# Kernel optimization log

Measured on AMD Instinct MI355X. Metric: run time of the kernel, lower is better.

## Reference

```python
import jax, jax.numpy as jnp
import numpy as np

# Dimensions (see shape_source): batch, tokens, input dim, attention feature dim, output dim
B, T, D_IN, D_ATTN, D_OUT = 8, 2048, 512, 8, 512
# Weight scale keeps Q,K entries ~N(0, 0.5^2) so scores**power stays finite in fp32
W_SCALE = 0.5 / np.sqrt(D_IN)


def setup_inputs() -> dict:
    key = jax.random.key(0)
    k1, k2, k3, k4 = jax.random.split(key, 4)
    Input = jax.random.normal(k1, (B, T, D_IN), dtype=jnp.float32)
    W_q = jax.random.normal(k2, (D_IN, D_ATTN), dtype=jnp.float32) * W_SCALE
    W_k = jax.random.normal(k3, (D_IN, D_ATTN), dtype=jnp.float32) * W_SCALE
    W_v = jax.random.normal(k4, (D_IN, D_OUT), dtype=jnp.float32) * W_SCALE
    return {"Input": Input, "W_q": W_q, "W_k": W_k, "W_v": W_v, "power": D_ATTN}


def reference(Input, W_q, W_k, W_v, power):
    # QKV projections (torch.mm applied per token)
    Q = jnp.einsum('btd,df->btf', Input, W_q)   # [B,T,D_ATTN]
    K = jnp.einsum('btd,df->btf', Input, W_k)   # [B,T,D_ATTN]
    V = jnp.einsum('btd,do->bto', Input, W_v)   # [B,T,D_OUT]
    # Non-standard score transform: elementwise power by Attention.Feature.Num
    scores = jnp.einsum('btf,bsf->bts', Q, K) ** power  # [B,T,T]
    A = jax.nn.softmax(scores, axis=2)
    # Weighted sum of values
    return jnp.einsum('bts,bso->bto', A, V)  # [B,T,D_OUT]
```

## Files before the change

### kernel.cpp

```cpp
#include <hip/hip_runtime.h>
#include <hip/hip_bf16.h>
#include <stdint.h>


typedef float f32x4_t __attribute__((ext_vector_type(4)));
typedef short s16x8_t __attribute__((ext_vector_type(8)));
typedef unsigned int u32;

static __device__ __forceinline__ unsigned short f2bf(float x){
  union { float f; u32 u; } v; v.f = x;
  return (unsigned short)((v.u + 0x7FFFu + ((v.u >> 16) & 1u)) >> 16);
}

static __device__ __forceinline__ u32 pk2bf(float a, float b){
  __hip_bfloat162 h = __float22bfloat162_rn(float2{a, b});
  union { __hip_bfloat162 h2; u32 u; } c; c.h2 = h;
  return c.u;
}

static __device__ __forceinline__ void gload16(const void* g, void* l){
  __builtin_amdgcn_global_load_lds((const __attribute__((address_space(1))) u32*)g,
                                   (__attribute__((address_space(3))) u32*)l, 16, 0, 0);
}

static __device__ __forceinline__ float dot8(const float* q, const float4& a, const float4& b){
  float s = q[0] * a.x;
  s = fmaf(q[1], a.y, s); s = fmaf(q[2], a.z, s); s = fmaf(q[3], a.w, s);
  s = fmaf(q[4], b.x, s); s = fmaf(q[5], b.y, s); s = fmaf(q[6], b.z, s);
  s = fmaf(q[7], b.w, s);
  return s;
}

__global__ __launch_bounds__(256) void k_wvT(const float* __restrict__ Wv,
                                             unsigned short* __restrict__ WvT){
  __shared__ __align__(16) float tile[64][68];
  const int t = threadIdx.x;
  const int dbase = (blockIdx.x >> 3) * 64;
  const int cbase = (blockIdx.x & 7) * 64;
  {
    const int dl = t >> 2, cq = (t & 3) * 16;
    const float* src = Wv + (size_t)(dbase + dl) * 512 + cbase + cq;
#pragma unroll
    for (int i = 0; i < 16; i += 4){
      float4 v = *(const float4*)(src + i);
      tile[dl][cq + i + 0] = v.x; tile[dl][cq + i + 1] = v.y;
      tile[dl][cq + i + 2] = v.z; tile[dl][cq + i + 3] = v.w;
    }
  }
  __syncthreads();
  const int cl = t >> 2, dq = (t & 3) * 16;
  __align__(16) unsigned short o[16];
#pragma unroll
  for (int i = 0; i < 16; ++i) o[i] = f2bf(tile[dq + i][cl]);
  unsigned short* dst = WvT + (size_t)(cbase + cl) * 512 + dbase + dq;
  *(uint4*)dst = *(const uint4*)o;
  *(uint4*)(dst + 8) = *(const uint4*)(o + 8);
}

__global__ __launch_bounds__(256) void k_fused(const float* __restrict__ In,
                                               const float* __restrict__ Wq,
                                               const float* __restrict__ Wk,
                                               const unsigned short* __restrict__ WvT,
                                               float* __restrict__ Qo,
                                               float* __restrict__ Ko,
                                               unsigned short* __restrict__ Vg){
  __shared__ __align__(16) char smem[65536];
  const int t = threadIdx.x;
  if (blockIdx.x < 1024){
    float* wt = (float*)smem;
    float* inT = (float*)(smem + 32768);
    const float* Inb = In + (size_t)blockIdx.x * 16 * 512;
#pragma unroll
    for (int i = 0; i < 8; ++i)
      gload16(Inb + (i * 256 + t) * 4, (char*)inT + (i * 256 + t) * 16);
#pragma unroll
    for (int i = 0; i < 16; i += 4){
      float4 vq = *(const float4*)(Wq + t * 16 + i);
      float4 vk = *(const float4*)(Wk + t * 16 + i);
      const float* pq = &vq.x;
      const float* pk = &vk.x;
#pragma unroll
      for (int j = 0; j < 4; ++j){
        int flat = t * 16 + i + j;
        int d = flat >> 3, f = flat & 7;
        wt[f * 512 + ((((d >> 2) ^ f) << 2) | (d & 3))] = pq[j];
        int fk = f + 8;
        wt[fk * 512 + ((((d >> 2) ^ (fk & 7)) << 2) | (d & 3))] = pk[j];
      }
    }
    __syncthreads();
    const int tokl = t >> 4;
    const int f = t & 15;
    const float* inrow = inT + tokl * 512;
    const float* wrow = &wt[f * 512];
    const int swz = f & 7;
    double acc = 0.0;
    for (int cb = 0; cb < 128; cb += 8){
      float part = 0.f;
#pragma unroll
      for (int c = cb; c < cb + 8; ++c){
        float4 x = *(const float4*)(inrow + c * 4);
        float4 ww = *(const float4*)(wrow + ((c ^ swz) << 2));
        part = fmaf(x.x, ww.x, part); part = fmaf(x.y, ww.y, part);
        part = fmaf(x.z, ww.z, part); part = fmaf(x.w, ww.w, part);
      }
      acc += (double)part;
    }
    float r = (float)acc;
    const int tok = (int)blockIdx.x * 16 + tokl;
    if (f < 8) Qo[(size_t)tok * 8 + f] = r;
    else       Ko[(size_t)tok * 8 + (f - 8)] = r;
    return;
  }
  char* Ab = smem;
  char* Bb = smem + 16384;
  char* Img = smem + 32768;
  const int vb = (int)blockIdx.x - 1024;
  const int w = t >> 6, lane = t & 63;
  const int mt = vb >> 2, nt = vb & 3;
  const int wm = w >> 1, wn = w & 1;
  const int asub = lane & 3;
  int arow[2], acr[2];
#pragma unroll
  for (int i = 0; i < 2; ++i){
    arow[i] = (w * 2 + i) * 16 + (lane >> 2);
    acr[i]  = asub ^ ((arow[i] >> 1) & 3);
  }
  f32x4_t acc[4][4];
#pragma unroll
  for (int m = 0; m < 4; ++m)
#pragma unroll
    for (int n = 0; n < 4; ++n)
      acc[m][n] = (f32x4_t){0.f, 0.f, 0.f, 0.f};

  auto stageB = [&](int kk, int sel){
#pragma unroll
    for (int i = 0; i < 2; ++i){
      int id = w * 2 + i;
      const unsigned short* gb = WvT + (size_t)(nt * 128 + arow[i]) * 512 + kk * 32 + acr[i] * 8;
      gload16(gb, Bb + sel * 8192 + id * 1024);
    }
  };
  auto loadA = [&](int kk, float4* x, float4* y){
#pragma unroll
    for (int i = 0; i < 2; ++i){
      const float* ga = In + (size_t)(mt * 128 + arow[i]) * 512 + kk * 32 + acr[i] * 8;
      x[i] = *(const float4*)ga;
      y[i] = *(const float4*)(ga + 4);
    }
  };
  auto writeA = [&](const float4* x, const float4* y, int sel){
#pragma unroll
    for (int i = 0; i < 2; ++i){
      __align__(16) unsigned short pk[8] = {
        f2bf(x[i].x), f2bf(x[i].y), f2bf(x[i].z), f2bf(x[i].w),
        f2bf(y[i].x), f2bf(y[i].y), f2bf(y[i].z), f2bf(y[i].w)};
      *(uint4*)(Ab + sel * 8192 + arow[i] * 64 + asub * 16) = *(const uint4*)pk;
    }
  };
  {
    float4 x[2], y[2];
    loadA(0, x, y);
    stageB(0, 0);
    writeA(x, y, 0);
    __syncthreads();
  }
  for (int kk = 0; kk < 16; ++kk){
    const int cur = kk & 1;
    float4 x[2], y[2];
    if (kk < 15){
      loadA(kk + 1, x, y);
      stageB(kk + 1, cur ^ 1);
    }
    s16x8_t a[4], bf[4];
#pragma unroll
    for (int m = 0; m < 4; ++m){
      int row = wm * 64 + m * 16 + (lane & 15);
      int chn = (lane >> 4) ^ ((row >> 1) & 3);
      a[m] = *(const s16x8_t*)(Ab + cur * 8192 + row * 64 + chn * 16);
    }
#pragma unroll
    for (int n = 0; n < 4; ++n){
      int col = wn * 64 + n * 16 + (lane & 15);
      int chn = (lane >> 4) ^ ((col >> 1) & 3);
      bf[n] = *(const s16x8_t*)(Bb + cur * 8192 + col * 64 + chn * 16);
    }
#pragma unroll
    for (int m = 0; m < 4; ++m)
#pragma unroll
      for (int n = 0; n < 4; ++n)
        acc[m][n] = __builtin_amdgcn_mfma_f32_16x16x32_bf16(a[m], bf[n], acc[m][n], 0, 0, 0);
    if (kk < 15) writeA(x, y, cur ^ 1);
    __syncthreads();
  }
#pragma unroll
  for (int m = 0; m < 4; ++m){
    const int ks2 = (wm * 2 + (m >> 1)) & 3;
    const int hi  = (m * 2 + ((lane >> 4) >> 1)) & 3;
    const int lo0 = ((lane >> 4) & 1) * 4;
#pragma unroll
    for (int n = 0; n < 4; ++n){
      const int g_loc = wn * 2 + (n >> 1);
      const int n2 = n & 1;
      const int cl = lane & 15;
      __align__(8) unsigned short pk2[4];
#pragma unroll
      for (int j = 0; j < 4; ++j) pk2[j] = f2bf(acc[m][n][j]);
      int boff = g_loc * 8192 + n2 * 4096 + ks2 * 1024 + hi * 256 + cl * 16 + lo0 * 2;
      *(uint2*)(Img + boff) = *(const uint2*)pk2;
    }
  }
  __syncthreads();
  const int bq = mt >> 4;
  const int kt = mt & 15;
#pragma unroll
  for (int i = 0; i < 8; ++i){
    int G = i * 256 + t;
    unsigned short* dst = Vg + (size_t)bq * 1048576 + (size_t)kt * 65536
                        + nt * 16384 + G * 8;
    *(uint4*)dst = *(const uint4*)(Img + G * 16);
  }
}

__global__ __launch_bounds__(1024) void k_attn(const float* __restrict__ Qg,
                                               const float* __restrict__ Kg,
                                               const unsigned short* __restrict__ Vg,
                                               float* __restrict__ Out){
  __shared__ __align__(16) char smem[102656];
  const int t = threadIdx.x;
  const int g = t >> 6, lane = t & 63;
  const int b = blockIdx.x & 7;
  const int qt = blockIdx.x >> 3;
  const int qbase = qt * 64;

  float qreg[8];
  {
    const float* Qp = Qg + (size_t)(b * 2048 + qbase + lane) * 8;
    float4 a = *(const float4*)Qp;
    float4 c = *(const float4*)(Qp + 4);
    qreg[0] = a.x; qreg[1] = a.y; qreg[2] = a.z; qreg[3] = a.w;
    qreg[4] = c.x; qreg[5] = c.y; qreg[6] = c.z; qreg[7] = c.w;
  }
  const float* Kp = Kg + (size_t)b * (2048 * 8);
  const unsigned short* Vb = Vg + (size_t)b * 1048576;
  char* Klds = smem;
  char* Pb = smem + 65536;
  float* red = (float*)(smem + 98304);
  float* fin = (float*)(smem + 102400);

#pragma unroll
  for (int i = 0; i < 4; ++i)
    gload16(Kp + (size_t)(i * 1024 + t) * 4, Klds + (i * 1024 + t) * 16);
  __syncthreads();

  float amax2 = 0.f;
  {
    const float* kbase = (const float*)Klds + (g * 8) * 8;
#pragma unroll 2
    for (int tt = 0; tt < 16; ++tt){
      const float* kb = kbase + tt * 1024;
#pragma unroll
      for (int j = 0; j < 8; ++j){
        float4 k0 = *(const float4*)(kb + j * 8);
        float4 k1 = *(const float4*)(kb + j * 8 + 4);
        float s = dot8(qreg, k0, k1);
        amax2 = fmaxf(amax2, s * s);
      }
    }
  }
  red[g * 64 + lane] = amax2;
  __syncthreads();
  float am = red[lane];
#pragma unroll
  for (int s = 1; s < 16; ++s) am = fmaxf(am, red[s * 64 + lane]);
  float mreg;
  { float s4 = am * am; mreg = s4 * s4; }
  const float LOG2E = 1.44269504f;
  const float me2 = mreg * LOG2E;
  float lp = 0.f;

  const int pswz = ((g ^ (lane & 15)) << 4);

  f32x4_t acc[4][2];
#pragma unroll
  for (int mm = 0; mm < 4; ++mm)
#pragma unroll
    for (int n = 0; n < 2; ++n)
      acc[mm][n] = (f32x4_t){0.f, 0.f, 0.f, 0.f};

  auto score_full = [&](int tt, int sel){
    const float* kb = (const float*)Klds + (tt * 128 + g * 8) * 8;
    uint4 pkd; u32* pw = &pkd.x;
#pragma unroll
    for (int jp = 0; jp < 4; ++jp){
      float e0, e1;
#pragma unroll
      for (int h = 0; h < 2; ++h){
        const int j = jp * 2 + h;
        float4 k0 = *(const float4*)(kb + j * 8);
        float4 k1 = *(const float4*)(kb + j * 8 + 4);
        float s = dot8(qreg, k0, k1);
        float s2 = s * s; float s4 = s2 * s2; float p = s4 * s4;
        float e = __builtin_amdgcn_exp2f(fmaf(p, LOG2E, -me2));
        lp += e;
        if (h == 0) e0 = e; else e1 = e;
      }
      pw[jp] = pk2bf(e0, e1);
    }
    *(uint4*)(Pb + sel * 16384 + lane * 256 + pswz) = pkd;
  };

  score_full(0, 0);
  __syncthreads();

  for (int tt = 0; tt < 16; ++tt){
    const int sel = tt & 1;
    s16x8_t vf[2][4];
    {
      const unsigned short* vb = Vb + (size_t)tt * 65536 + g * 4096 + lane * 8;
#pragma unroll
      for (int n = 0; n < 2; ++n)
#pragma unroll
        for (int ks = 0; ks < 4; ++ks)
          vf[n][ks] = *(const s16x8_t*)(vb + n * 2048 + ks * 512);
    }
    const bool more = (tt + 1 < 16);
    const float* kb = (const float*)Klds + (((tt + 1) & 15) * 128 + g * 8) * 8;
    uint4 pkd; u32* pw = &pkd.x;
#pragma unroll
    for (int ks = 0; ks < 4; ++ks){
      if (more){
        float e0, e1;
#pragma unroll
        for (int h = 0; h < 2; ++h){
          const int j = ks * 2 + h;
          float4 k0 = *(const float4*)(kb + j * 8);
          float4 k1 = *(const float4*)(kb + j * 8 + 4);
          float s = dot8(qreg, k0, k1);
          float s2 = s * s; float s4 = s2 * s2; float p = s4 * s4;
          float e = __builtin_amdgcn_exp2f(fmaf(p, LOG2E, -me2));
          lp += e;
          if (h == 0) e0 = e; else e1 = e;
        }
        pw[ks] = pk2bf(e0, e1);
      }
      s16x8_t a[4];
#pragma unroll
      for (int mm = 0; mm < 4; ++mm){
        int r = mm * 16 + (lane & 15);
        int slot = (ks * 4 + (lane >> 4)) ^ (r & 15);
        a[mm] = *(const s16x8_t*)(Pb + sel * 16384 + r * 256 + (slot << 4));
      }
      __builtin_amdgcn_s_setprio(1);
#pragma unroll
      for (int mm = 0; mm < 4; ++mm)
#pragma unroll
        for (int n = 0; n < 2; ++n)
          acc[mm][n] = __builtin_amdgcn_mfma_f32_16x16x32_bf16(a[mm], vf[n][ks], acc[mm][n], 0, 0, 0);
      __builtin_amdgcn_s_setprio(0);
    }
    if (more)
      *(uint4*)(Pb + (sel ^ 1) * 16384 + lane * 256 + pswz) = pkd;
    __syncthreads();
  }

  red[g * 64 + lane] = lp;
  __syncthreads();
  if (t < 64){
    float s = red[t];
#pragma unroll
    for (int s2 = 1; s2 < 16; ++s2) s += red[s2 * 64 + t];
    fin[t] = 1.f / s;
  }
  __syncthreads();

  float* img = (float*)smem;
#pragma unroll
  for (int mm = 0; mm < 4; ++mm){
    float linv[4];
#pragma unroll
    for (int j = 0; j < 4; ++j)
      linv[j] = fin[mm * 16 + ((lane >> 4) << 2) + j];
#pragma unroll
    for (int n = 0; n < 2; ++n){
      int colL = g * 32 + n * 16 + (lane & 15);
#pragma unroll
      for (int j = 0; j < 4; ++j){
        int r16 = ((lane >> 4) << 2) + j;
        img[r16 * 520 + colL] = acc[mm][n][j] * linv[j];
      }
    }
    __syncthreads();
#pragma unroll
    for (int i = 0; i < 2; ++i){
      int f4 = i * 1024 + t;
      int r16 = f4 >> 7, c4 = f4 & 127;
      float4 v = *(const float4*)(img + r16 * 520 + c4 * 4);
      *(float4*)(Out + (size_t)(b * 2048 + qbase + mm * 16 + r16) * 512 + c4 * 4) = v;
    }
    __syncthreads();
  }
}

extern "C" void kernel_launch(void* const* d_in, const int* in_sizes, int n_in,
                              void* d_out, int out_size, void* d_ws, size_t ws_size,
                              hipStream_t stream){
  const float* In = (const float*)d_in[0];
  const float* Wq = (const float*)d_in[1];
  const float* Wk = (const float*)d_in[2];
  const float* Wv = (const float*)d_in[3];
  char* ws = (char*)d_ws;
  unsigned short* WvT = (unsigned short*)(ws);
  float* Q            = (float*)(ws + 524288);
  float* K            = (float*)(ws + 1048576);
  unsigned short* Vg  = (unsigned short*)(ws + 1572864);
  float* Out = (float*)d_out;

  hipLaunchKernelGGL(k_wvT,   dim3(64),   dim3(256),  0, stream, Wv, WvT);
  hipLaunchKernelGGL(k_fused, dim3(1536), dim3(256),  0, stream, In, Wq, Wk, WvT, Q, K, Vg);
  hipLaunchKernelGGL(k_attn,  dim3(256),  dim3(1024), 0, stream, Q, K, Vg, Out);
}
```

Measured before the change: 99.17 us.

## Transpose K layout and vectorize score computation with packed FMA

The projection kernel now writes K in a feature-major tiled layout of 128 keys per tile, so each attention lane can read four consecutive keys per feature with one float4 LDS load. Scores are then computed two keys at a time using packed f32x2 FMAs (v_pk_fma_f32), and the power, exp-argument and row-sum steps are vectorized the same way. The intent is to cut VALU instruction count and LDS load count in the score-bound inner loop. Score computation is regrouped into two calls per tile instead of one per k-step, which changes how it interleaves with the MFMAs.

```diff
diff --git a/kernel.cpp b/kernel.cpp
--- a/kernel.cpp
+++ b/kernel.cpp
@@ -4,6 +4,7 @@
 
 
 typedef float f32x4_t __attribute__((ext_vector_type(4)));
+typedef float f32x2_t __attribute__((ext_vector_type(2)));
 typedef short s16x8_t __attribute__((ext_vector_type(8)));
 typedef unsigned int u32;
 
@@ -23,12 +24,8 @@
                                    (__attribute__((address_space(3))) u32*)l, 16, 0, 0);
 }
 
-static __device__ __forceinline__ float dot8(const float* q, const float4& a, const float4& b){
-  float s = q[0] * a.x;
-  s = fmaf(q[1], a.y, s); s = fmaf(q[2], a.z, s); s = fmaf(q[3], a.w, s);
-  s = fmaf(q[4], b.x, s); s = fmaf(q[5], b.y, s); s = fmaf(q[6], b.z, s);
-  s = fmaf(q[7], b.w, s);
-  return s;
+static __device__ __forceinline__ f32x2_t pfma(f32x2_t a, f32x2_t b, f32x2_t c){
+  return __builtin_elementwise_fma(a, b, c);
 }
 
 __global__ __launch_bounds__(256) void k_wvT(const float* __restrict__ Wv,
@@ -62,7 +59,7 @@
                                                const float* __restrict__ Wk,
                                                const unsigned short* __restrict__ WvT,
                                                float* __restrict__ Qo,
-                                               float* __restrict__ Ko,
+                                               float* __restrict__ Kt,
                                                unsigned short* __restrict__ Vg){
   __shared__ __align__(16) char smem[65536];
   const int t = threadIdx.x;
@@ -109,7 +106,10 @@
     float r = (float)acc;
     const int tok = (int)blockIdx.x * 16 + tokl;
     if (f < 8) Qo[(size_t)tok * 8 + f] = r;
-    else       Ko[(size_t)tok * 8 + (f - 8)] = r;
+    else {
+      const int bq = tok >> 11, kk = tok & 2047;
+      Kt[(size_t)bq * 16384 + (size_t)(kk >> 7) * 1024 + (f - 8) * 128 + (kk & 127)] = r;
+    }
     return;
   }
   char* Ab = smem;
@@ -223,7 +223,7 @@
 }
 
 __global__ __launch_bounds__(1024) void k_attn(const float* __restrict__ Qg,
-                                               const float* __restrict__ Kg,
+                                               const float* __restrict__ Kt,
                                                const unsigned short* __restrict__ Vg,
                                                float* __restrict__ Out){
   __shared__ __align__(16) char smem[102656];
@@ -233,15 +233,17 @@
   const int qt = blockIdx.x >> 3;
   const int qbase = qt * 64;
 
-  float qreg[8];
+  f32x2_t qq[8];
   {
     const float* Qp = Qg + (size_t)(b * 2048 + qbase + lane) * 8;
     float4 a = *(const float4*)Qp;
     float4 c = *(const float4*)(Qp + 4);
-    qreg[0] = a.x; qreg[1] = a.y; qreg[2] = a.z; qreg[3] = a.w;
-    qreg[4] = c.x; qreg[5] = c.y; qreg[6] = c.z; qreg[7] = c.w;
-  }
-  const float* Kp = Kg + (size_t)b * (2048 * 8);
+    qq[0] = (f32x2_t){a.x, a.x}; qq[1] = (f32x2_t){a.y, a.y};
+    qq[2] = (f32x2_t){a.z, a.z}; qq[3] = (f32x2_t){a.w, a.w};
+    qq[4] = (f32x2_t){c.x, c.x}; qq[5] = (f32x2_t){c.y, c.y};
+    qq[6] = (f32x2_t){c.z, c.z}; qq[7] = (f32x2_t){c.w, c.w};
+  }
+  const float* Kp = Kt + (size_t)b * 16384;
   const unsigned short* Vb = Vg + (size_t)b * 1048576;
   char* Klds = smem;
   char* Pb = smem + 65536;
@@ -255,16 +257,21 @@
 
   float amax2 = 0.f;
   {
-    const float* kbase = (const float*)Klds + (g * 8) * 8;
+    const float* kbase = (const float*)Klds + g * 8;
 #pragma unroll 2
     for (int tt = 0; tt < 16; ++tt){
       const float* kb = kbase + tt * 1024;
 #pragma unroll
-      for (int j = 0; j < 8; ++j){
-        float4 k0 = *(const float4*)(kb + j * 8);
-        float4 k1 = *(const float4*)(kb + j * 8 + 4);
-        float s = dot8(qreg, k0, k1);
-        amax2 = fmaxf(amax2, s * s);
+      for (int j = 0; j < 2; ++j){
+        f32x2_t p0 = {0.f, 0.f}, p1 = {0.f, 0.f};
+#pragma unroll
+        for (int d = 0; d < 8; ++d){
+          float4 v = *(const float4*)(kb + d * 128 + j * 4);
+          p0 = pfma(qq[d], (f32x2_t){v.x, v.y}, p0);
+          p1 = pfma(qq[d], (f32x2_t){v.z, v.w}, p1);
+        }
+        f32x2_t s0 = p0 * p0, s1 = p1 * p1;
+        amax2 = fmaxf(amax2, fmaxf(fmaxf(s0.x, s0.y), fmaxf(s1.x, s1.y)));
       }
     }
   }
@@ -276,8 +283,9 @@
   float mreg;
   { float s4 = am * am; mreg = s4 * s4; }
   const float LOG2E = 1.44269504f;
-  const float me2 = mreg * LOG2E;
-  float lp = 0.f;
+  const f32x2_t l2e  = (f32x2_t){LOG2E, LOG2E};
+  const f32x2_t nme2 = (f32x2_t){-mreg * LOG2E, -mreg * LOG2E};
+  f32x2_t lpp = (f32x2_t){0.f, 0.f};
 
   const int pswz = ((g ^ (lane & 15)) << 4);
 
@@ -288,29 +296,33 @@
     for (int n = 0; n < 2; ++n)
       acc[mm][n] = (f32x4_t){0.f, 0.f, 0.f, 0.f};
 
-  auto score_full = [&](int tt, int sel){
-    const float* kb = (const float*)Klds + (tt * 128 + g * 8) * 8;
-    uint4 pkd; u32* pw = &pkd.x;
-#pragma unroll
-    for (int jp = 0; jp < 4; ++jp){
-      float e0, e1;
-#pragma unroll
-      for (int h = 0; h < 2; ++h){
-        const int j = jp * 2 + h;
-        float4 k0 = *(const float4*)(kb + j * 8);
-        float4 k1 = *(const float4*)(kb + j * 8 + 4);
-        float s = dot8(qreg, k0, k1);
-        float s2 = s * s; float s4 = s2 * s2; float p = s4 * s4;
-        float e = __builtin_amdgcn_exp2f(fmaf(p, LOG2E, -me2));
-        lp += e;
-        if (h == 0) e0 = e; else e1 = e;
-      }
-      pw[jp] = pk2bf(e0, e1);
-    }
-    *(uint4*)(Pb + sel * 16384 + lane * 256 + pswz) = pkd;
+  auto score4 = [&](const float* kb, int j, u32* pw){
+    f32x2_t p0 = {0.f, 0.f}, p1 = {0.f, 0.f};
+#pragma unroll
+    for (int d = 0; d < 8; ++d){
+      float4 v = *(const float4*)(kb + d * 128 + j * 4);
+      p0 = pfma(qq[d], (f32x2_t){v.x, v.y}, p0);
+      p1 = pfma(qq[d], (f32x2_t){v.z, v.w}, p1);
+    }
+    p0 = p0 * p0; p1 = p1 * p1;
+    p0 = p0 * p0; p1 = p1 * p1;
+    p0 = p0 * p0; p1 = p1 * p1;
+    p0 = pfma(p0, l2e, nme2); p1 = pfma(p1, l2e, nme2);
+    float e0 = __builtin_amdgcn_exp2f(p0.x), e1 = __builtin_amdgcn_exp2f(p0.y);
+    float e2 = __builtin_amdgcn_exp2f(p1.x), e3 = __builtin_amdgcn_exp2f(p1.y);
+    lpp += (f32x2_t){e0, e1};
+    lpp += (f32x2_t){e2, e3};
+    pw[0] = pk2bf(e0, e1);
+    pw[1] = pk2bf(e2, e3);
   };
 
-  score_full(0, 0);
+  {
+    const float* kb0 = (const float*)Klds + g * 8;
+    uint4 pkd;
+    score4(kb0, 0, &pkd.x);
+    score4(kb0, 1, &pkd.z);
+    *(uint4*)(Pb + 0 * 16384 + lane * 256 + pswz) = pkd;
+  }
   __syncthreads();
 
   for (int tt = 0; tt < 16; ++tt){
@@ -325,25 +337,12 @@
           vf[n][ks] = *(const s16x8_t*)(vb + n * 2048 + ks * 512);
     }
     const bool more = (tt + 1 < 16);
-    const float* kb = (const float*)Klds + (((tt + 1) & 15) * 128 + g * 8) * 8;
-    uint4 pkd; u32* pw = &pkd.x;
+    const float* kbn = (const float*)Klds + ((tt + 1) & 15) * 1024 + g * 8;
+    uint4 pkd;
 #pragma unroll
     for (int ks = 0; ks < 4; ++ks){
-      if (more){
-        float e0, e1;
-#pragma unroll
-        for (int h = 0; h < 2; ++h){
-          const int j = ks * 2 + h;
-          float4 k0 = *(const float4*)(kb + j * 8);
-          float4 k1 = *(const float4*)(kb + j * 8 + 4);
-          float s = dot8(qreg, k0, k1);
-          float s2 = s * s; float s4 = s2 * s2; float p = s4 * s4;
-          float e = __builtin_amdgcn_exp2f(fmaf(p, LOG2E, -me2));
-          lp += e;
-          if (h == 0) e0 = e; else e1 = e;
-        }
-        pw[ks] = pk2bf(e0, e1);
-      }
+      if (more && ks == 0) score4(kbn, 0, &pkd.x);
+      if (more && ks == 2) score4(kbn, 1, &pkd.z);
       s16x8_t a[4];
 #pragma unroll
       for (int mm = 0; mm < 4; ++mm){
@@ -364,7 +363,7 @@
     __syncthreads();
   }
 
-  red[g * 64 + lane] = lp;
+  red[g * 64 + lane] = lpp.x + lpp.y;
   __syncthreads();
   if (t < 64){
     float s = red[t];
@@ -412,11 +411,11 @@
   char* ws = (char*)d_ws;
   unsigned short* WvT = (unsigned short*)(ws);
   float* Q            = (float*)(ws + 524288);
-  float* K            = (float*)(ws + 1048576);
+  float* Kt           = (float*)(ws + 1048576);
   unsigned short* Vg  = (unsigned short*)(ws + 1572864);
   float* Out = (float*)d_out;
 
   hipLaunchKernelGGL(k_wvT,   dim3(64),   dim3(256),  0, stream, Wv, WvT);
-  hipLaunchKernelGGL(k_fused, dim3(1536), dim3(256),  0, stream, In, Wq, Wk, WvT, Q, K, Vg);
-  hipLaunchKernelGGL(k_attn,  dim3(256),  dim3(1024), 0, stream, Q, K, Vg, Out);
-}
+  hipLaunchKernelGGL(k_fused, dim3(1536), dim3(256),  0, stream, In, Wq, Wk, WvT, Q, Kt, Vg);
+  hipLaunchKernelGGL(k_attn,  dim3(256),  dim3(1024), 0, stream, Q, Kt, Vg, Out);
+}
```

After: 100.2 us. Within noise of the previous version (+1.1%).
